# Kernel tuning notes

Measured on AMD Instinct MI355X. Metric: run time of the kernel, lower is better.

## Reference

```python
import jax, jax.numpy as jnp
import numpy as np

N = 500000
IN_C = 128
OUT_C = 128


def setup_inputs() -> dict:
    key = jax.random.key(0)
    k1, k2, k3, k4 = jax.random.split(key, 4)
    x = jax.random.normal(k1, (N, IN_C), dtype=jnp.float32)
    # E must equal N for the original `out + out[col]` broadcast to be valid
    edge_index = jax.random.randint(k2, (2, N), 0, N, dtype=jnp.int64)
    # Linear(in_channels, out_channels): W [out, in], b [out]
    bound = 1.0 / np.sqrt(IN_C)
    W = jax.random.uniform(k3, (OUT_C, IN_C), dtype=jnp.float32, minval=-bound, maxval=bound)
    b = jax.random.uniform(k4, (OUT_C,), dtype=jnp.float32, minval=-bound, maxval=bound)
    return {"x": x, "edge_index": edge_index, "W": W, "b": b}


def reference(x, edge_index, W, b):
    row, col = edge_index[0], edge_index[1]
    out = x @ W.T + b                      # [N, C] dense projection
    # gather rows by col, then scatter-add +1 at positions row (duplicates accumulate)
    agg = out[col].at[row].add(jnp.float32(1.0))  # [E, C], E == N
    return out + agg
```

## Files before the change

kernel.cpp:

```cpp
#include <hip/hip_runtime.h>
#include <hip/hip_bf16.h>
#include <stdint.h>

typedef __attribute__((ext_vector_type(8))) __bf16 bf16x8;
typedef __attribute__((ext_vector_type(4))) float floatx4;

#define C 128
#define BROWS 64
#define LSTR 136

__device__ __forceinline__ __bf16 f2b(float f) {
  return __builtin_bit_cast(__bf16, __float2bfloat16(f));
}

__global__ void zero_kernel(int* __restrict__ p, int n) {
  int i = blockIdx.x * blockDim.x + threadIdx.x;
  if (i < n) p[i] = 0;
}

__global__ void prep_kernel(const int* __restrict__ rowidx, const float* __restrict__ W,
                            int* __restrict__ deg, __bf16* __restrict__ Wb, int n) {
  int i = blockIdx.x * blockDim.x + threadIdx.x;
  if (i < C * C) Wb[i] = f2b(W[i]);
  if (i < n) atomicAdd(deg + rowidx[i], 1);
}

__launch_bounds__(256, 3)
__global__ void gconv_kernel(const float* __restrict__ x,
                             const int* __restrict__ colidx,
                             const __bf16* __restrict__ Wb,
                             const float* __restrict__ bias,
                             const int* __restrict__ deg,
                             float* __restrict__ out, int n) {
  __shared__ __bf16 sIn[BROWS * LSTR];
  __shared__ __bf16 sW[C * LSTR];
  __shared__ float sDeg[BROWS];

  const int t = threadIdx.x;
  const int base = blockIdx.x * BROWS;

  {
    int r = t >> 1, h = t & 1;
    const float4* src = (const float4*)(Wb + r * C + h * 64);
    float4* dst = (float4*)(sW + r * LSTR + h * 64);
#pragma unroll
    for (int i = 0; i < 8; i++) dst[i] = src[i];
  }
  if (t < BROWS) {
    int g = base + t;
    sDeg[t] = (g < n) ? (float)deg[g] : 0.0f;
  }
  {
    int r = t >> 2, q = t & 3;
    int g = base + r;
    if (g < n) {
      int cg = colidx[g];
      const float4* p0 = (const float4*)(x + (size_t)g * C + q * 32);
      const float4* p1 = (const float4*)(x + (size_t)cg * C + q * 32);
      __bf16* drow = sIn + r * LSTR + q * 32;
#pragma unroll
      for (int i = 0; i < 4; i++) {
        float4 a0 = p0[2 * i], a1 = p0[2 * i + 1];
        float4 c0 = p1[2 * i], c1 = p1[2 * i + 1];
        bf16x8 u;
        u[0] = f2b(a0.x + c0.x); u[1] = f2b(a0.y + c0.y);
        u[2] = f2b(a0.z + c0.z); u[3] = f2b(a0.w + c0.w);
        u[4] = f2b(a1.x + c1.x); u[5] = f2b(a1.y + c1.y);
        u[6] = f2b(a1.z + c1.z); u[7] = f2b(a1.w + c1.w);
        *(bf16x8*)(drow + i * 8) = u;
      }
    }
  }
  __syncthreads();

  const int lane = t & 63, w = t >> 6;
  const int l15 = lane & 15, quad = lane >> 4;

  floatx4 acc[8];
#pragma unroll
  for (int i = 0; i < 8; i++) acc[i] = (floatx4){0.f, 0.f, 0.f, 0.f};

  const __bf16* aB = sIn + (w * 16 + l15) * LSTR + quad * 8;
  const __bf16* bB = sW + l15 * LSTR + quad * 8;

#pragma unroll
  for (int kc = 0; kc < 4; kc++) {
    bf16x8 av = *(const bf16x8*)(aB + kc * 32);
#pragma unroll
    for (int tt = 0; tt < 8; tt++) {
      bf16x8 bv = *(const bf16x8*)(bB + tt * 16 * LSTR + kc * 32);
      acc[tt] = __builtin_amdgcn_mfma_f32_16x16x32_bf16(av, bv, acc[tt], 0, 0, 0);
    }
  }

  float degv[4];
#pragma unroll
  for (int r = 0; r < 4; r++) degv[r] = sDeg[w * 16 + quad * 4 + r];

#pragma unroll
  for (int tt = 0; tt < 8; tt++) {
    int ncol = tt * 16 + l15;
    float b2 = 2.0f * bias[ncol];
#pragma unroll
    for (int r = 0; r < 4; r++) {
      int g = base + w * 16 + quad * 4 + r;
      if (g < n) out[(size_t)g * C + ncol] = acc[tt][r] + b2 + degv[r];
    }
  }
}

extern "C" void kernel_launch(void* const* d_in, const int* in_sizes, int n_in,
                              void* d_out, int out_size, void* d_ws, size_t ws_size,
                              hipStream_t stream) {
  const float* x    = (const float*)d_in[0];
  const int*   edge = (const int*)d_in[1];
  const float* W    = (const float*)d_in[2];
  const float* bias = (const float*)d_in[3];
  float* out = (float*)d_out;

  const int n = in_sizes[0] / C;

  int* deg = (int*)d_ws;
  size_t wb_off = ((size_t)n * sizeof(int) + 255) & ~(size_t)255;
  __bf16* Wb = (__bf16*)((char*)d_ws + wb_off);

  int nb = (n + 255) / 256;
  zero_kernel<<<nb, 256, 0, stream>>>(deg, n);
  prep_kernel<<<nb, 256, 0, stream>>>(edge, W, deg, Wb, n);

  int mb = (n + BROWS - 1) / BROWS;
  gconv_kernel<<<mb, 256, 0, stream>>>(x, edge + n, Wb, bias, deg, out, n);
}
```

Before: 540.1 us.

## Use persistent blocks that load A operands directly into registers

The GEMM kernel becomes persistent with a capped grid. Each block stages W in LDS once and loops over row tiles. The summed x rows are loaded straight from global memory into MFMA operand registers, removing the LDS staging buffer and the per-tile barrier, and the next tile's column index is prefetched. The changes aim to cut the W reload per tile, the LDS traffic and the synchronization, and allow higher occupancy. The trade-off is more register pressure and uncoalesced per-lane global loads of x.

New measurement: 589.1 us. +9.1%, slower.

```diff
diff --git a/kernel.cpp b/kernel.cpp
--- a/kernel.cpp
+++ b/kernel.cpp
@@ -25,19 +25,16 @@
   if (i < n) atomicAdd(deg + rowidx[i], 1);
 }
 
-__launch_bounds__(256, 3)
+__launch_bounds__(256, 4)
 __global__ void gconv_kernel(const float* __restrict__ x,
                              const int* __restrict__ colidx,
                              const __bf16* __restrict__ Wb,
                              const float* __restrict__ bias,
                              const int* __restrict__ deg,
-                             float* __restrict__ out, int n) {
-  __shared__ __bf16 sIn[BROWS * LSTR];
+                             float* __restrict__ out, int n, int ntiles) {
   __shared__ __bf16 sW[C * LSTR];
-  __shared__ float sDeg[BROWS];
 
   const int t = threadIdx.x;
-  const int base = blockIdx.x * BROWS;
 
   {
     int r = t >> 1, h = t & 1;
@@ -46,66 +43,82 @@
 #pragma unroll
     for (int i = 0; i < 8; i++) dst[i] = src[i];
   }
-  if (t < BROWS) {
-    int g = base + t;
-    sDeg[t] = (g < n) ? (float)deg[g] : 0.0f;
-  }
-  {
-    int r = t >> 2, q = t & 3;
-    int g = base + r;
-    if (g < n) {
-      int cg = colidx[g];
-      const float4* p0 = (const float4*)(x + (size_t)g * C + q * 32);
-      const float4* p1 = (const float4*)(x + (size_t)cg * C + q * 32);
-      __bf16* drow = sIn + r * LSTR + q * 32;
-#pragma unroll
-      for (int i = 0; i < 4; i++) {
-        float4 a0 = p0[2 * i], a1 = p0[2 * i + 1];
-        float4 c0 = p1[2 * i], c1 = p1[2 * i + 1];
-        bf16x8 u;
-        u[0] = f2b(a0.x + c0.x); u[1] = f2b(a0.y + c0.y);
-        u[2] = f2b(a0.z + c0.z); u[3] = f2b(a0.w + c0.w);
-        u[4] = f2b(a1.x + c1.x); u[5] = f2b(a1.y + c1.y);
-        u[6] = f2b(a1.z + c1.z); u[7] = f2b(a1.w + c1.w);
-        *(bf16x8*)(drow + i * 8) = u;
-      }
-    }
-  }
-  __syncthreads();
 
   const int lane = t & 63, w = t >> 6;
   const int l15 = lane & 15, quad = lane >> 4;
 
-  floatx4 acc[8];
+  float b2[8];
 #pragma unroll
-  for (int i = 0; i < 8; i++) acc[i] = (floatx4){0.f, 0.f, 0.f, 0.f};
+  for (int tt = 0; tt < 8; tt++) b2[tt] = 2.0f * bias[tt * 16 + l15];
 
-  const __bf16* aB = sIn + (w * 16 + l15) * LSTR + quad * 8;
+  __syncthreads();
+
   const __bf16* bB = sW + l15 * LSTR + quad * 8;
 
+  int tile = blockIdx.x;
+
+  int ga  = tile * BROWS + w * 16 + l15;
+  int gal = ga < n ? ga : n - 1;
+  int cg  = colidx[gal];
+
+  for (; tile < ntiles; tile += gridDim.x) {
+    const int base = tile * BROWS + w * 16;
+
+    const float4* pa = (const float4*)(x + (size_t)gal * C + quad * 8);
+    const float4* pc = (const float4*)(x + (size_t)cg  * C + quad * 8);
+    float4 va[8], vc[8];
 #pragma unroll
-  for (int kc = 0; kc < 4; kc++) {
-    bf16x8 av = *(const bf16x8*)(aB + kc * 32);
+    for (int kc = 0; kc < 4; kc++) {
+      va[2 * kc]     = pa[kc * 8];
+      va[2 * kc + 1] = pa[kc * 8 + 1];
+      vc[2 * kc]     = pc[kc * 8];
+      vc[2 * kc + 1] = pc[kc * 8 + 1];
+    }
+
+    int gr  = base + quad * 4;
+    int grl = (gr + 3 < n) ? gr : ((n - 4) & ~3);
+    int4 d4 = *(const int4*)(deg + grl);
+
+    int ntile = tile + gridDim.x;
+    int nga   = ntile * BROWS + w * 16 + l15;
+    int ngal  = (ntile < ntiles) ? (nga < n ? nga : n - 1) : gal;
+    int ncg   = colidx[ngal];
+
+    floatx4 acc[8];
 #pragma unroll
-    for (int tt = 0; tt < 8; tt++) {
-      bf16x8 bv = *(const bf16x8*)(bB + tt * 16 * LSTR + kc * 32);
-      acc[tt] = __builtin_amdgcn_mfma_f32_16x16x32_bf16(av, bv, acc[tt], 0, 0, 0);
-    }
-  }
-
-  float degv[4];
-#pragma unroll
-  for (int r = 0; r < 4; r++) degv[r] = sDeg[w * 16 + quad * 4 + r];
+    for (int i = 0; i < 8; i++) acc[i] = (floatx4){0.f, 0.f, 0.f, 0.f};
 
 #pragma unroll
-  for (int tt = 0; tt < 8; tt++) {
-    int ncol = tt * 16 + l15;
-    float b2 = 2.0f * bias[ncol];
+    for (int kc = 0; kc < 4; kc++) {
+      float4 a0 = va[2 * kc], a1 = va[2 * kc + 1];
+      float4 c0 = vc[2 * kc], c1 = vc[2 * kc + 1];
+      bf16x8 av;
+      av[0] = f2b(a0.x + c0.x); av[1] = f2b(a0.y + c0.y);
+      av[2] = f2b(a0.z + c0.z); av[3] = f2b(a0.w + c0.w);
+      av[4] = f2b(a1.x + c1.x); av[5] = f2b(a1.y + c1.y);
+      av[6] = f2b(a1.z + c1.z); av[7] = f2b(a1.w + c1.w);
+#pragma unroll
+      for (int tt = 0; tt < 8; tt++) {
+        bf16x8 bv = *(const bf16x8*)(bB + tt * 16 * LSTR + kc * 32);
+        acc[tt] = __builtin_amdgcn_mfma_f32_16x16x32_bf16(av, bv, acc[tt], 0, 0, 0);
+      }
+    }
+
+    float dvf[4];
+    dvf[0] = (float)d4.x; dvf[1] = (float)d4.y;
+    dvf[2] = (float)d4.z; dvf[3] = (float)d4.w;
 #pragma unroll
     for (int r = 0; r < 4; r++) {
-      int g = base + w * 16 + quad * 4 + r;
-      if (g < n) out[(size_t)g * C + ncol] = acc[tt][r] + b2 + degv[r];
+      int g = gr + r;
+      if (g < n) {
+        float* orow = out + (size_t)g * C + l15;
+        float dv = dvf[r];
+#pragma unroll
+        for (int tt = 0; tt < 8; tt++) orow[tt * 16] = acc[tt][r] + b2[tt] + dv;
+      }
     }
+
+    gal = ngal; cg = ncg;
   }
 }
 
@@ -128,6 +141,7 @@
   zero_kernel<<<nb, 256, 0, stream>>>(deg, n);
   prep_kernel<<<nb, 256, 0, stream>>>(edge, W, deg, Wb, n);
 
-  int mb = (n + BROWS - 1) / BROWS;
-  gconv_kernel<<<mb, 256, 0, stream>>>(x, edge + n, Wb, bias, deg, out, n);
+  int ntiles = (n + BROWS - 1) / BROWS;
+  int blocks = ntiles < 2048 ? ntiles : 2048;
+  gconv_kernel<<<blocks, 256, 0, stream>>>(x, edge + n, Wb, bias, deg, out, n, ntiles);
 }
```
